# Optimization experiments

Measured on AMD Instinct MI355X. Metric: run time of the kernel, lower is better.

The kernel has to match this reference:

```python
import jax, jax.numpy as jnp
import numpy as np

EMBED = 1024
HEADS = 16
HEAD_DIM = EMBED // HEADS
HIDDEN = 4096
EPS = 1e-5


def setup_inputs() -> dict:
    key = jax.random.key(0)
    ks = jax.random.split(key, 12)
    s_e = 1.0 / np.sqrt(EMBED)
    s_h = 1.0 / np.sqrt(HIDDEN)
    inp = {
        'x': jax.random.normal(ks[0], (2, 2048, EMBED), jnp.float32),
        'Wq': jax.random.uniform(ks[1], (EMBED, EMBED), jnp.float32, -s_e, s_e),
        'bq': jnp.zeros((EMBED,), jnp.float32),
        'Wk': jax.random.uniform(ks[2], (EMBED, EMBED), jnp.float32, -s_e, s_e),
        'bk': jnp.zeros((EMBED,), jnp.float32),
        'Wv': jax.random.uniform(ks[3], (EMBED, EMBED), jnp.float32, -s_e, s_e),
        'bv': jnp.zeros((EMBED,), jnp.float32),
        'Wo': jax.random.uniform(ks[4], (EMBED, EMBED), jnp.float32, -s_e, s_e),
        'bo': jnp.zeros((EMBED,), jnp.float32),
        'g1': jnp.ones((EMBED,), jnp.float32),
        'b1': jnp.zeros((EMBED,), jnp.float32),
        'W1': jax.random.uniform(ks[5], (EMBED, HIDDEN), jnp.float32, -s_e, s_e),
        'bm1': jnp.zeros((HIDDEN,), jnp.float32),
        'W2': jax.random.uniform(ks[6], (HIDDEN, EMBED), jnp.float32, -s_h, s_h),
        'bm2': jnp.zeros((EMBED,), jnp.float32),
        'g2': jnp.ones((EMBED,), jnp.float32),
        'b2': jnp.zeros((EMBED,), jnp.float32),
    }
    return inp


def _layernorm(x, g, b):
    mu = jnp.mean(x, axis=-1, keepdims=True)
    var = jnp.mean(jnp.square(x - mu), axis=-1, keepdims=True)
    return (x - mu) * jax.lax.rsqrt(var + EPS) * g + b


def _attention(x, Wq, bq, Wk, bk, Wv, bv, Wo, bo):
    b, n, d = x.shape
    def split(h):  # [b,n,d] -> [b,H,n,hd]
        return h.reshape(b, n, HEADS, HEAD_DIM).transpose(0, 2, 1, 3)
    q = split(x @ Wq + bq)
    k = split(x @ Wk + bk)
    v = split(x @ Wv + bv)
    # NOTE: original multiplies by sqrt(head_dim) (bug preserved for faithfulness)
    scores = jnp.einsum('bhqd,bhkd->bhqk', q, k) * jnp.sqrt(jnp.float32(HEAD_DIM))
    causal = jnp.tril(jnp.ones((n, n), bool))
    scores = jnp.where(causal, scores, -jnp.inf)
    attn = jax.nn.softmax(scores, axis=-1)
    out = jnp.einsum('bhqk,bhkd->bhqd', attn, v)
    out = out.transpose(0, 2, 1, 3).reshape(b, n, d)
    return out @ Wo + bo


def reference(x, Wq, bq, Wk, bk, Wv, bv, Wo, bo, g1, b1, W1, bm1, W2, bm2, g2, b2):
    res1 = x
    x = _layernorm(_attention(x, Wq, bq, Wk, bk, Wv, bv, Wo, bo), g1, b1) + res1
    res2 = x
    h = jax.nn.gelu(x @ W1 + bm1, approximate=False) @ W2 + bm2
    return _layernorm(h, g2, b2) + res2
```

## Files before the change

kernel.cpp:

```cpp
#include <hip/hip_runtime.h>
#include <stdint.h>

typedef unsigned short u16;
typedef short short8 __attribute__((ext_vector_type(8)));
typedef float f32x4 __attribute__((ext_vector_type(4)));
typedef u16 u16x4 __attribute__((ext_vector_type(4)));
typedef u16 u16x8 __attribute__((ext_vector_type(8)));

#define MODE_F32  0
#define MODE_GELU 2
#define MODE_VT   4

#define QSCALE 11.5415603271f

__device__ __forceinline__ float b2f(u16 v) {
    union { uint32_t u; float f; } x; x.u = ((uint32_t)v) << 16; return x.f;
}
__device__ __forceinline__ u16 f2b(float f) {
    union { float f; uint32_t u; } x; x.f = f;
    uint32_t u = x.u;
    return (u16)((u + 0x7FFFu + ((u >> 16) & 1u)) >> 16);
}
__device__ __forceinline__ u16 f2b_trunc(float f) {
    union { float f; uint32_t u; } x; x.f = f;
    return (u16)(x.u >> 16);
}

#define ASYNC16(gp, lp)                                                        \
    __builtin_amdgcn_global_load_lds(                                          \
        (const __attribute__((address_space(1))) uint32_t*)(const void*)(gp),  \
        (__attribute__((address_space(3))) uint32_t*)(void*)(lp), 16, 0, 0)

#define MFMA16(a, b, c) __builtin_amdgcn_mfma_f32_16x16x32_bf16((a), (b), (c), 0, 0, 0)

__global__ __launch_bounds__(256) void split_f32(
    const float* __restrict__ in, u16* __restrict__ hi, u16* __restrict__ lo)
{
    const int i = (blockIdx.x * 256 + threadIdx.x) * 4;
    f32x4 v = *(const f32x4*)&in[i];
    u16x4 h, l;
    for (int k = 0; k < 4; k++) {
        h[k] = f2b(v[k]);
        l[k] = f2b(v[k] - b2f(h[k]));
    }
    *(u16x4*)&hi[i] = h;
    *(u16x4*)&lo[i] = l;
}

__global__ __launch_bounds__(256) void transpose_f32_bf16(
    const float* __restrict__ inA, u16* __restrict__ outA,
    const float* __restrict__ inB, u16* __restrict__ outB, int rows, int cols)
{
    const float* in = blockIdx.z ? inB : inA;
    u16* out = blockIdx.z ? outB : outA;
    __shared__ float t[32][33];
    const int r0 = blockIdx.y * 32, c0 = blockIdx.x * 32;
    const int tr = threadIdx.x >> 3, tc = (threadIdx.x & 7) * 4;
    f32x4 v = *(const f32x4*)&in[(size_t)(r0 + tr) * cols + c0 + tc];
    for (int i = 0; i < 4; i++) t[tr][tc + i] = v[i];
    __syncthreads();
    u16x4 ov;
    for (int i = 0; i < 4; i++) ov[i] = f2b(t[tc + i][tr]);
    *(u16x4*)&out[(size_t)(c0 + tr) * rows + r0 + tc] = ov;
}

__global__ __launch_bounds__(256) void transpose_split_f32(
    const float* __restrict__ inA, u16* __restrict__ hiA, u16* __restrict__ loA,
    const float* __restrict__ inB, u16* __restrict__ hiB, u16* __restrict__ loB,
    int rows, int cols)
{
    const float* in = blockIdx.z ? inB : inA;
    u16* hi = blockIdx.z ? hiB : hiA;
    u16* lo = blockIdx.z ? loB : loA;
    __shared__ float t[32][33];
    const int r0 = blockIdx.y * 32, c0 = blockIdx.x * 32;
    const int tr = threadIdx.x >> 3, tc = (threadIdx.x & 7) * 4;
    f32x4 v = *(const f32x4*)&in[(size_t)(r0 + tr) * cols + c0 + tc];
    for (int i = 0; i < 4; i++) t[tr][tc + i] = v[i];
    __syncthreads();
    u16x4 hv, lv;
    for (int i = 0; i < 4; i++) {
        const float f = t[tc + i][tr];
        hv[i] = f2b(f);
        lv[i] = f2b(f - b2f(hv[i]));
    }
    const size_t o = (size_t)(c0 + tr) * rows + r0 + tc;
    *(u16x4*)&hi[o] = hv;
    *(u16x4*)&lo[o] = lv;
}

__global__ __launch_bounds__(256) void gemm_qk_x3(
    const u16* __restrict__ Ahi, const u16* __restrict__ Alo,
    const u16* __restrict__ Bhi, const u16* __restrict__ Blo,
    const float* __restrict__ bq, const float* __restrict__ bk,
    u16* __restrict__ Qhi, u16* __restrict__ Qlo,
    u16* __restrict__ Khi, u16* __restrict__ Klo)
{
    const int K = 1024;
    __shared__ __align__(16) u16 SM[32768];
    u16* lAh = SM;          u16* lAl = SM + 8192;
    u16* lBh = SM + 16384;  u16* lBl = SM + 24576;

    const int tid = threadIdx.x;
    const int w = tid >> 6, lane = tid & 63;
    const int lane15 = lane & 15, q = lane >> 4;
    const int tM = blockIdx.y * 128, tN = blockIdx.x * 128;
    const int m0 = (w >> 1) * 64, n0 = (w & 1) * 64;

    f32x4 acc[4][4];
    for (int i = 0; i < 4; i++)
        for (int j = 0; j < 4; j++)
            acc[i][j] = (f32x4){0.f, 0.f, 0.f, 0.f};

    const int pa0 = 2 * w, pa1 = 2 * w + 1;
    const int srow = lane >> 2, sch = lane & 3;
    const u16* Ah = Ahi + (size_t)tM * K;
    const u16* Al = Alo + (size_t)tM * K;
    const u16* Bh = Bhi + (size_t)tN * K;
    const u16* Bl = Blo + (size_t)tN * K;
    const size_t r0 = (size_t)(pa0 * 16 + srow) * K + sch * 8;
    const size_t r1 = (size_t)(pa1 * 16 + srow) * K + sch * 8;

    ASYNC16(Ah + r0, lAh + pa0 * 512);  ASYNC16(Ah + r1, lAh + pa1 * 512);
    ASYNC16(Al + r0, lAl + pa0 * 512);  ASYNC16(Al + r1, lAl + pa1 * 512);
    ASYNC16(Bh + r0, lBh + pa0 * 512);  ASYNC16(Bh + r1, lBh + pa1 * 512);
    ASYNC16(Bl + r0, lBl + pa0 * 512);  ASYNC16(Bl + r1, lBl + pa1 * 512);

    const int NT = K / 32;
    for (int kt = 0; kt < NT; kt++) {
        __syncthreads();
        const int cb = (kt & 1) * 4096, nb = 4096 - cb;
        if (kt + 1 < NT) {
            const int k0 = (kt + 1) * 32;
            ASYNC16(Ah + r0 + k0, lAh + nb + pa0 * 512);  ASYNC16(Ah + r1 + k0, lAh + nb + pa1 * 512);
            ASYNC16(Al + r0 + k0, lAl + nb + pa0 * 512);  ASYNC16(Al + r1 + k0, lAl + nb + pa1 * 512);
            ASYNC16(Bh + r0 + k0, lBh + nb + pa0 * 512);  ASYNC16(Bh + r1 + k0, lBh + nb + pa1 * 512);
            ASYNC16(Bl + r0 + k0, lBl + nb + pa0 * 512);  ASYNC16(Bl + r1 + k0, lBl + nb + pa1 * 512);
        }
        short8 afh[4], afl[4], bfh[4], bfl[4];
        for (int i = 0; i < 4; i++) {
            const int o = cb + (m0 + i * 16 + lane15) * 32 + q * 8;
            afh[i] = *(const short8*)&lAh[o];
            afl[i] = *(const short8*)&lAl[o];
        }
        for (int j = 0; j < 4; j++) {
            const int o = cb + (n0 + j * 16 + lane15) * 32 + q * 8;
            bfh[j] = *(const short8*)&lBh[o];
            bfl[j] = *(const short8*)&lBl[o];
        }
        for (int i = 0; i < 4; i++)
            for (int j = 0; j < 4; j++) {
                acc[i][j] = MFMA16(afh[i], bfh[j], acc[i][j]);
                acc[i][j] = MFMA16(afh[i], bfl[j], acc[i][j]);
                acc[i][j] = MFMA16(afl[i], bfh[j], acc[i][j]);
            }
    }

    const bool isQ = (tN < 1024);
    u16* dhi = isQ ? Qhi : Khi;
    u16* dlo = isQ ? Qlo : Klo;
    const int cN = isQ ? tN : (tN - 1024);
    const float scl = isQ ? QSCALE : 1.0f;
    u16* sC = SM;
    for (int pass = 0; pass < 2; pass++) {
        __syncthreads();
        for (int i = 0; i < 4; i++) {
            const int rl0 = m0 + i * 16 + q * 4;
            for (int j = 0; j < 4; j++) {
                const int cl = n0 + j * 16 + lane15;
                const float bv = isQ ? bq[cN + cl] : bk[cN + cl];
                for (int r = 0; r < 4; r++) {
                    const float v = (acc[i][j][r] + bv) * scl;
                    const u16 hv = f2b(v);
                    sC[(rl0 + r) * 136 + cl] = pass == 0 ? hv : f2b(v - b2f(hv));
                }
            }
        }
        __syncthreads();
        u16* dst = pass == 0 ? dhi : dlo;
        for (int t8 = 0; t8 < 8; t8++) {
            const int rl = t8 * 16 + (tid >> 4), cl = (tid & 15) * 8;
            *(u16x8*)&dst[(size_t)(tM + rl) * 1024 + cN + cl] = *(const u16x8*)&sC[rl * 136 + cl];
        }
    }
}

__global__ __launch_bounds__(256) void gemm_bt(
    const u16* __restrict__ A, const u16* __restrict__ Bt, const float* __restrict__ bias,
    int M, int N, int K, int mode,
    float* __restrict__ outF, u16* __restrict__ outB, size_t pstride)
{
    __shared__ __align__(16) u16 SM[17408];
    u16* lA = SM;
    u16* lB = SM + 8192;

    const int tid = threadIdx.x;
    const int w = tid >> 6, lane = tid & 63;
    const int lane15 = lane & 15, q = lane >> 4;
    const int tM = blockIdx.y * 128, tN = blockIdx.x * 128;
    const int m0 = (w >> 1) * 64, n0 = (w & 1) * 64;

    const int kchunk = K / gridDim.z;
    const int koff = blockIdx.z * kchunk;
    outF += (size_t)blockIdx.z * pstride;

    f32x4 acc[4][4];
    for (int i = 0; i < 4; i++)
        for (int j = 0; j < 4; j++)
            acc[i][j] = (f32x4){0.f, 0.f, 0.f, 0.f};

    const int pa0 = 2 * w, pa1 = 2 * w + 1;
    const int srow = lane >> 2, sch = lane & 3;
    const u16* Abase = A + (size_t)tM * K + koff;
    const u16* Bbase = Bt + (size_t)tN * K + koff;
    const size_t r0 = (size_t)(pa0 * 16 + srow) * K + sch * 8;
    const size_t r1 = (size_t)(pa1 * 16 + srow) * K + sch * 8;

    ASYNC16(Abase + r0, lA + pa0 * 512);
    ASYNC16(Abase + r1, lA + pa1 * 512);
    ASYNC16(Bbase + r0, lB + pa0 * 512);
    ASYNC16(Bbase + r1, lB + pa1 * 512);

    const int NT = kchunk / 32;
    for (int kt = 0; kt < NT; kt++) {
        __syncthreads();
        const int cb = (kt & 1) * 4096, nb = 4096 - cb;
        if (kt + 1 < NT) {
            const int k0 = (kt + 1) * 32;
            ASYNC16(Abase + r0 + k0, lA + nb + pa0 * 512);
            ASYNC16(Abase + r1 + k0, lA + nb + pa1 * 512);
            ASYNC16(Bbase + r0 + k0, lB + nb + pa0 * 512);
            ASYNC16(Bbase + r1 + k0, lB + nb + pa1 * 512);
        }
        short8 af[4], bf[4];
        for (int i = 0; i < 4; i++) af[i] = *(const short8*)&lA[cb + (m0 + i * 16 + lane15) * 32 + q * 8];
        for (int j = 0; j < 4; j++) bf[j] = *(const short8*)&lB[cb + (n0 + j * 16 + lane15) * 32 + q * 8];
        for (int i = 0; i < 4; i++)
            for (int j = 0; j < 4; j++)
                acc[i][j] = MFMA16(af[i], bf[j], acc[i][j]);
    }

    if (mode == MODE_F32) {
        for (int i = 0; i < 4; i++) {
            const int rb = tM + m0 + i * 16 + q * 4;
            for (int j = 0; j < 4; j++) {
                const int col = tN + n0 + j * 16 + lane15;
                const float bv = (bias && blockIdx.z == 0) ? bias[col] : 0.f;
                for (int r = 0; r < 4; r++)
                    outF[(size_t)(rb + r) * N + col] = acc[i][j][r] + bv;
            }
        }
        return;
    }

    u16* sC = SM;
    __syncthreads();
    if (mode == MODE_GELU) {
        for (int i = 0; i < 4; i++) {
            const int rl0 = m0 + i * 16 + q * 4;
            for (int j = 0; j < 4; j++) {
                const int cl = n0 + j * 16 + lane15;
                const float bv = bias[tN + cl];
                for (int r = 0; r < 4; r++) {
                    float v = acc[i][j][r] + bv;
                    v = 0.5f * v * (1.f + erff(v * 0.70710678118f));
                    sC[(rl0 + r) * 136 + cl] = f2b(v);
                }
            }
        }
        __syncthreads();
        for (int t8 = 0; t8 < 8; t8++) {
            const int rl = t8 * 16 + (tid >> 4), cl = (tid & 15) * 8;
            *(u16x8*)&outB[(size_t)(tM + rl) * N + tN + cl] = *(const u16x8*)&sC[rl * 136 + cl];
        }
    } else {
        for (int i = 0; i < 4; i++) {
            const int rl0 = m0 + i * 16 + q * 4;
            for (int j = 0; j < 4; j++) {
                const int cl = n0 + j * 16 + lane15;
                const float bv = bias[tN + cl];
                for (int r = 0; r < 4; r++)
                    sC[cl * 136 + rl0 + r] = f2b(acc[i][j][r] + bv);
            }
        }
        __syncthreads();
        const int bb = tM >> 11, nbase = tM & 2047;
        for (int t8 = 0; t8 < 8; t8++) {
            const int cl = t8 * 16 + (tid >> 4), rl = (tid & 15) * 8;
            const int colg = tN + cl;
            u16* dst = &outB[((size_t)(bb * 16 + (colg >> 6)) * 64 + (colg & 63)) * 2048 + nbase + rl];
            *(u16x8*)dst = *(const u16x8*)&sC[cl * 136 + rl];
        }
    }
}

__global__ __launch_bounds__(256) void attn_fwd(
    const u16* __restrict__ Qhig, const u16* __restrict__ Qlog,
    const u16* __restrict__ Khig, const u16* __restrict__ Klog,
    const u16* __restrict__ Vtg, u16* __restrict__ Og)
{
    __shared__ u16 lQh[2][2048], lQl[2][2048];
    __shared__ u16 lKh[2][2][1024], lKl[2][2][1024];
    __shared__ u16 lV[2][2048];

    const int tid = threadIdx.x, w = tid >> 6, lane = tid & 63;
    const int lane15 = lane & 15, q = lane >> 4;
    const int bh = blockIdx.x & 31;
    const int qb = 31 - (blockIdx.x >> 5);
    const int b = bh >> 4, h = bh & 15;

    const size_t xoff = (size_t)b * 2048 * 1024 + h * 64;
    const u16* Qh_ = Qhig + xoff;
    const u16* Ql_ = Qlog + xoff;
    const u16* Kh_ = Khig + xoff;
    const u16* Kl_ = Klog + xoff;
    const u16* Vbh = Vtg + (size_t)bh * 64 * 2048;
    u16* Obh = Og + xoff;

    u16* lP = &lQh[0][0] + w * 640;

    const int srow = lane >> 2, sch = lane & 3;
    const float NEG = -3.0e38f;
    const int qrow0 = qb * 64;
    const int wrow0 = qrow0 + w * 16;
    const int ntiles = 2 * qb + 2;

    short8 ones;
    for (int i = 0; i < 8; i++) ones[i] = (short)0x3F80;

    for (int ii = 0; ii < 4; ii++) {
        const int id = w * 4 + ii;
        const int idq = id & 7, ks = idq >> 2, p = idq & 3;
        const size_t so = (size_t)(qrow0 + p * 16 + srow) * 1024 + ks * 32 + sch * 8;
        if (id < 8) ASYNC16(Qh_ + so, &lQh[ks][p * 512]);
        else        ASYNC16(Ql_ + so, &lQl[ks][p * 512]);
    }
    for (int ii = 0; ii < 3; ii++) {
        const int id = w * 3 + ii;
        if (id < 8) {
            const int sel = id >> 2, idk = id & 3, ks = idk >> 1, hh = idk & 1;
            const size_t so = (size_t)(hh * 16 + srow) * 1024 + ks * 32 + sch * 8;
            if (sel == 0) ASYNC16(Kh_ + so, &lKh[0][ks][hh * 512]);
            else          ASYNC16(Kl_ + so, &lKl[0][ks][hh * 512]);
        } else {
            const int p = id - 8;
            ASYNC16(Vbh + (size_t)(p * 16 + srow) * 2048 + sch * 8, &lV[0][p * 512]);
        }
    }

    f32x4 o[4];
    for (int j = 0; j < 4; j++) o[j] = (f32x4){0.f, 0.f, 0.f, 0.f};
    float mrow[4], lrow[4];
    for (int r = 0; r < 4; r++) { mrow[r] = NEG; lrow[r] = 0.f; }
    short8 aqh0 = {}, aqh1 = {}, aql0 = {}, aql1 = {};

    for (int t = 0; t < ntiles; t++) {
        __syncthreads();
        const int cur = t & 1, nxt = cur ^ 1;
        if (t == 0) {
            const int o0 = (w * 16 + lane15) * 32 + q * 8;
            aqh0 = *(const short8*)&lQh[0][o0];
            aqh1 = *(const short8*)&lQh[1][o0];
            aql0 = *(const short8*)&lQl[0][o0];
            aql1 = *(const short8*)&lQl[1][o0];
            __syncthreads();
        }
        if (t + 1 < ntiles) {
            const int kk1 = (t + 1) * 32;
            for (int ii = 0; ii < 3; ii++) {
                const int id = w * 3 + ii;
                if (id < 8) {
                    const int sel = id >> 2, idk = id & 3, ks = idk >> 1, hh = idk & 1;
                    const size_t so = (size_t)(kk1 + hh * 16 + srow) * 1024 + ks * 32 + sch * 8;
                    if (sel == 0) ASYNC16(Kh_ + so, &lKh[nxt][ks][hh * 512]);
                    else          ASYNC16(Kl_ + so, &lKl[nxt][ks][hh * 512]);
                } else {
                    const int p = id - 8;
                    ASYNC16(Vbh + (size_t)(p * 16 + srow) * 2048 + kk1 + sch * 8,
                            &lV[nxt][p * 512]);
                }
            }
        }
        const int kk0 = t * 32;
        if (kk0 > wrow0 + 15) continue;

        f32x4 s[2];
        for (int sub = 0; sub < 2; sub++) {
            const int ko = (sub * 16 + lane15) * 32 + q * 8;
            short8 bkh0 = *(const short8*)&lKh[cur][0][ko];
            short8 bkh1 = *(const short8*)&lKh[cur][1][ko];
            short8 bkl0 = *(const short8*)&lKl[cur][0][ko];
            short8 bkl1 = *(const short8*)&lKl[cur][1][ko];
            f32x4 z = (f32x4){0.f, 0.f, 0.f, 0.f};
            z = MFMA16(aqh0, bkh0, z);
            z = MFMA16(aqh1, bkh1, z);
            z = MFMA16(aqh0, bkl0, z);
            z = MFMA16(aqh1, bkl1, z);
            z = MFMA16(aql0, bkh0, z);
            z = MFMA16(aql1, bkh1, z);
            s[sub] = z;
        }
        const int rbase = wrow0 + q * 4;
        if (kk0 + 31 > wrow0) {
            for (int sub = 0; sub < 2; sub++)
                for (int r = 0; r < 4; r++) {
                    const int key = kk0 + sub * 16 + lane15;
                    if (key > rbase + r) s[sub][r] = NEG;
                }
        }
        float mx[4];
        for (int r = 0; r < 4; r++) mx[r] = fmaxf(s[0][r], s[1][r]);
        for (int d = 1; d < 16; d <<= 1)
            for (int r = 0; r < 4; r++) mx[r] = fmaxf(mx[r], __shfl_xor(mx[r], d));
        float alpha[4];
        for (int r = 0; r < 4; r++) {
            const float mnew = fmaxf(mrow[r], mx[r]);
            alpha[r] = __builtin_exp2f(mrow[r] - mnew);
            mrow[r] = mnew;
        }
        for (int sub = 0; sub < 2; sub++)
            for (int r = 0; r < 4; r++) {
                const float p = __builtin_exp2f(s[sub][r] - mrow[r]);
                lP[(q * 4 + r) * 40 + sub * 16 + lane15] = f2b_trunc(p);
            }
        short8 ap = *(const short8*)&lP[lane15 * 40 + q * 8];
        f32x4 zs = (f32x4){0.f, 0.f, 0.f, 0.f};
        zs = MFMA16(ap, ones, zs);
        for (int r = 0; r < 4; r++) lrow[r] = lrow[r] * alpha[r] + zs[r];
        for (int j = 0; j < 4; j++)
            for (int r = 0; r < 4; r++) o[j][r] *= alpha[r];
        for (int j = 0; j < 4; j++) {
            short8 bv = *(const short8*)&lV[cur][(j * 16 + lane15) * 32 + q * 8];
            o[j] = MFMA16(ap, bv, o[j]);
        }
    }
    float inv[4];
    for (int r = 0; r < 4; r++) inv[r] = 1.0f / lrow[r];
    for (int j = 0; j < 4; j++)
        for (int r = 0; r < 4; r++)
            Obh[(size_t)(qrow0 + w * 16 + q * 4 + r) * 1024 + j * 16 + lane15] =
                f2b(o[j][r] * inv[r]);
}

__global__ __launch_bounds__(256) void ln_res(
    const float* __restrict__ Xa, const float* __restrict__ Xb,
    const float* __restrict__ resF, const u16* __restrict__ resB,
    const float* __restrict__ g, const float* __restrict__ bb,
    u16* __restrict__ outB, float* __restrict__ outF)
{
    const int w = threadIdx.x >> 6, lane = threadIdx.x & 63;
    const int row = blockIdx.x * 4 + w;
    const size_t rowo = (size_t)row * 1024;
    f32x4 v[4];
    float s = 0.f, ss = 0.f;
    for (int i = 0; i < 4; i++) {
        const int c0 = (i * 64 + lane) * 4;
        v[i] = *(const f32x4*)&Xa[rowo + c0];
        if (Xb) {
            f32x4 v2 = *(const f32x4*)&Xb[rowo + c0];
            for (int k = 0; k < 4; k++) v[i][k] += v2[k];
        }
        for (int k = 0; k < 4; k++) { s += v[i][k]; ss += v[i][k] * v[i][k]; }
    }
    for (int d = 1; d < 64; d <<= 1) { s += __shfl_xor(s, d); ss += __shfl_xor(ss, d); }
    const float mu = s * (1.f / 1024.f);
    const float var = ss * (1.f / 1024.f) - mu * mu;
    const float rstd = rsqrtf(var + 1e-5f);
    for (int i = 0; i < 4; i++) {
        const int c0 = (i * 64 + lane) * 4;
        f32x4 gv = *(const f32x4*)&g[c0];
        f32x4 bv = *(const f32x4*)&bb[c0];
        f32x4 rv;
        if (resF) rv = *(const f32x4*)&resF[rowo + c0];
        else {
            u16x4 rb = *(const u16x4*)&resB[rowo + c0];
            for (int k = 0; k < 4; k++) rv[k] = b2f(rb[k]);
        }
        f32x4 ov;
        for (int k = 0; k < 4; k++)
            ov[k] = (v[i][k] - mu) * rstd * gv[k] + bv[k] + rv[k];
        if (outF) *(f32x4*)&outF[rowo + c0] = ov;
        if (outB) {
            u16x4 ob;
            for (int k = 0; k < 4; k++) ob[k] = f2b(ov[k]);
            *(u16x4*)&outB[rowo + c0] = ob;
        }
    }
}

extern "C" void kernel_launch(void* const* d_in, const int* in_sizes, int n_in,
                              void* d_out, int out_size, void* d_ws, size_t ws_size,
                              hipStream_t stream)
{
    const float* x   = (const float*)d_in[0];
    const float* Wq  = (const float*)d_in[1];  const float* bq  = (const float*)d_in[2];
    const float* Wk  = (const float*)d_in[3];  const float* bk  = (const float*)d_in[4];
    const float* Wv  = (const float*)d_in[5];  const float* bv  = (const float*)d_in[6];
    const float* Wo  = (const float*)d_in[7];  const float* bo  = (const float*)d_in[8];
    const float* g1  = (const float*)d_in[9];  const float* b1  = (const float*)d_in[10];
    const float* W1  = (const float*)d_in[11]; const float* bm1 = (const float*)d_in[12];
    const float* W2  = (const float*)d_in[13]; const float* bm2 = (const float*)d_in[14];
    const float* g2  = (const float*)d_in[15]; const float* b2  = (const float*)d_in[16];

    const size_t MB = (size_t)1 << 20;
    char* ws = (char*)d_ws;
    u16* xhi    = (u16*)(ws + 0 * MB);
    u16* xlo    = (u16*)(ws + 8 * MB);
    u16* WqkThi = (u16*)(ws + 16 * MB);
    u16* WqkTlo = (u16*)(ws + 20 * MB);
    u16* WvT    = (u16*)(ws + 24 * MB);
    u16* WoT    = (u16*)(ws + 26 * MB);
    u16* W1T    = (u16*)(ws + 32 * MB);
    u16* W2T    = (u16*)(ws + 40 * MB);
    u16* Qhi    = (u16*)(ws + 48 * MB);
    u16* Qlo    = (u16*)(ws + 56 * MB);
    u16* Khi    = (u16*)(ws + 64 * MB);
    u16* Klo    = (u16*)(ws + 72 * MB);
    u16* Vtb    = (u16*)(ws + 80 * MB);
    u16* aout   = (u16*)(ws + 16 * MB);
    float* O1   = (float*)(ws + 48 * MB);
    float* O2   = (float*)(ws + 64 * MB);
    u16* x1b    = (u16*)(ws + 80 * MB);
    u16* Hb     = (u16*)(ws + 0 * MB);
    float* H2a  = (float*)(ws + 48 * MB);
    float* H2b  = (float*)(ws + 64 * MB);

    split_f32<<<4096, 256, 0, stream>>>(x, xhi, xlo);
    transpose_split_f32<<<dim3(32, 32, 2), 256, 0, stream>>>(
        Wq, WqkThi, WqkTlo,
        Wk, WqkThi + 1024 * 1024, WqkTlo + 1024 * 1024, 1024, 1024);
    transpose_f32_bf16<<<dim3(32, 32, 2), 256, 0, stream>>>(Wv, WvT, Wo, WoT, 1024, 1024);
    transpose_f32_bf16<<<dim3(128, 32), 256, 0, stream>>>(W1, W1T, nullptr, nullptr, 1024, 4096);
    transpose_f32_bf16<<<dim3(32, 128), 256, 0, stream>>>(W2, W2T, nullptr, nullptr, 4096, 1024);

    gemm_qk_x3<<<dim3(16, 32), 256, 0, stream>>>(xhi, xlo, WqkThi, WqkTlo, bq, bk,
                                                 Qhi, Qlo, Khi, Klo);
    gemm_bt<<<dim3(8, 32), 256, 0, stream>>>(xhi, WvT, bv, 4096, 1024, 1024,
                                             MODE_VT, nullptr, Vtb, 0);

    attn_fwd<<<dim3(1024), 256, 0, stream>>>(Qhi, Qlo, Khi, Klo, Vtb, aout);

    gemm_bt<<<dim3(8, 32, 2), 256, 0, stream>>>(aout, WoT, bo, 4096, 1024, 1024,
                                                MODE_F32, O1, nullptr, (size_t)16 * MB / 4);
    ln_res<<<1024, 256, 0, stream>>>(O1, O2, x, nullptr, g1, b1, x1b, nullptr);

    gemm_bt<<<dim3(32, 32), 256, 0, stream>>>(x1b, W1T, bm1, 4096, 4096, 1024,
                                              MODE_GELU, nullptr, Hb, 0);
    gemm_bt<<<dim3(8, 32, 2), 256, 0, stream>>>(Hb, W2T, bm2, 4096, 1024, 4096,
                                                MODE_F32, H2a, nullptr, (size_t)16 * MB / 4);
    ln_res<<<1024, 256, 0, stream>>>(H2a, H2b, nullptr, x1b, g2, b2, nullptr, (float*)d_out);
}
```

Baseline: 472.0 us.

## Use 8 waves per 128x128 GEMM tile and interleave attention block order

Both GEMM kernels now launch 512 threads per block, each wave owning a 32x64 sub-tile instead of 64x64. The global-to-LDS staging is redistributed across the eight waves. This halves accumulator registers per thread and doubles the waves available to hide latency, at the cost of more LDS fragment reads per MFMA. Separately, attention blocks alternate long and short causal query rows so heavy and light work items are interleaved across the grid, aiming at better load balance.

```diff
diff --git a/kernel.cpp b/kernel.cpp
--- a/kernel.cpp
+++ b/kernel.cpp
@@ -89,7 +89,7 @@
     *(u16x4*)&lo[o] = lv;
 }
 
-__global__ __launch_bounds__(256) void gemm_qk_x3(
+__global__ __launch_bounds__(512) void gemm_qk_x3(
     const u16* __restrict__ Ahi, const u16* __restrict__ Alo,
     const u16* __restrict__ Bhi, const u16* __restrict__ Blo,
     const float* __restrict__ bq, const float* __restrict__ bk,
@@ -105,26 +105,30 @@
     const int w = tid >> 6, lane = tid & 63;
     const int lane15 = lane & 15, q = lane >> 4;
     const int tM = blockIdx.y * 128, tN = blockIdx.x * 128;
-    const int m0 = (w >> 1) * 64, n0 = (w & 1) * 64;
-
-    f32x4 acc[4][4];
-    for (int i = 0; i < 4; i++)
+    const int m0 = (w >> 1) * 32, n0 = (w & 1) * 64;
+
+    f32x4 acc[2][4];
+    for (int i = 0; i < 2; i++)
         for (int j = 0; j < 4; j++)
             acc[i][j] = (f32x4){0.f, 0.f, 0.f, 0.f};
 
-    const int pa0 = 2 * w, pa1 = 2 * w + 1;
     const int srow = lane >> 2, sch = lane & 3;
     const u16* Ah = Ahi + (size_t)tM * K;
     const u16* Al = Alo + (size_t)tM * K;
     const u16* Bh = Bhi + (size_t)tN * K;
     const u16* Bl = Blo + (size_t)tN * K;
-    const size_t r0 = (size_t)(pa0 * 16 + srow) * K + sch * 8;
-    const size_t r1 = (size_t)(pa1 * 16 + srow) * K + sch * 8;
-
-    ASYNC16(Ah + r0, lAh + pa0 * 512);  ASYNC16(Ah + r1, lAh + pa1 * 512);
-    ASYNC16(Al + r0, lAl + pa0 * 512);  ASYNC16(Al + r1, lAl + pa1 * 512);
-    ASYNC16(Bh + r0, lBh + pa0 * 512);  ASYNC16(Bh + r1, lBh + pa1 * 512);
-    ASYNC16(Bl + r0, lBl + pa0 * 512);  ASYNC16(Bl + r1, lBl + pa1 * 512);
+    const size_t roff = (size_t)((w * 4) & 7) * 16 * K;
+
+    #define STAGE_QK(buf_off, k0)                                              \
+        for (int ii = 0; ii < 4; ii++) {                                       \
+            const int id = w * 4 + ii, op = id >> 3, ch = id & 7;              \
+            const u16* src = op == 0 ? Ah : op == 1 ? Al : op == 2 ? Bh : Bl;  \
+            u16* dst = op == 0 ? lAh : op == 1 ? lAl : op == 2 ? lBh : lBl;    \
+            ASYNC16(src + (size_t)(ch * 16 + srow) * K + (k0) + sch * 8,       \
+                    dst + (buf_off) + ch * 512);                               \
+        }
+
+    STAGE_QK(0, 0)
 
     const int NT = K / 32;
     for (int kt = 0; kt < NT; kt++) {
@@ -132,13 +136,10 @@
         const int cb = (kt & 1) * 4096, nb = 4096 - cb;
         if (kt + 1 < NT) {
             const int k0 = (kt + 1) * 32;
-            ASYNC16(Ah + r0 + k0, lAh + nb + pa0 * 512);  ASYNC16(Ah + r1 + k0, lAh + nb + pa1 * 512);
-            ASYNC16(Al + r0 + k0, lAl + nb + pa0 * 512);  ASYNC16(Al + r1 + k0, lAl + nb + pa1 * 512);
-            ASYNC16(Bh + r0 + k0, lBh + nb + pa0 * 512);  ASYNC16(Bh + r1 + k0, lBh + nb + pa1 * 512);
-            ASYNC16(Bl + r0 + k0, lBl + nb + pa0 * 512);  ASYNC16(Bl + r1 + k0, lBl + nb + pa1 * 512);
-        }
-        short8 afh[4], afl[4], bfh[4], bfl[4];
-        for (int i = 0; i < 4; i++) {
+            STAGE_QK(nb, k0)
+        }
+        short8 afh[2], afl[2], bfh[4], bfl[4];
+        for (int i = 0; i < 2; i++) {
             const int o = cb + (m0 + i * 16 + lane15) * 32 + q * 8;
             afh[i] = *(const short8*)&lAh[o];
             afl[i] = *(const short8*)&lAl[o];
@@ -148,7 +149,7 @@
             bfh[j] = *(const short8*)&lBh[o];
             bfl[j] = *(const short8*)&lBl[o];
         }
-        for (int i = 0; i < 4; i++)
+        for (int i = 0; i < 2; i++)
             for (int j = 0; j < 4; j++) {
                 acc[i][j] = MFMA16(afh[i], bfh[j], acc[i][j]);
                 acc[i][j] = MFMA16(afh[i], bfl[j], acc[i][j]);
@@ -164,7 +165,7 @@
     u16* sC = SM;
     for (int pass = 0; pass < 2; pass++) {
         __syncthreads();
-        for (int i = 0; i < 4; i++) {
+        for (int i = 0; i < 2; i++) {
             const int rl0 = m0 + i * 16 + q * 4;
             for (int j = 0; j < 4; j++) {
                 const int cl = n0 + j * 16 + lane15;
@@ -178,14 +179,14 @@
         }
         __syncthreads();
         u16* dst = pass == 0 ? dhi : dlo;
-        for (int t8 = 0; t8 < 8; t8++) {
-            const int rl = t8 * 16 + (tid >> 4), cl = (tid & 15) * 8;
+        for (int t8 = 0; t8 < 4; t8++) {
+            const int rl = t8 * 32 + (tid >> 4), cl = (tid & 15) * 8;
             *(u16x8*)&dst[(size_t)(tM + rl) * 1024 + cN + cl] = *(const u16x8*)&sC[rl * 136 + cl];
         }
     }
 }
 
-__global__ __launch_bounds__(256) void gemm_bt(
+__global__ __launch_bounds__(512) void gemm_bt(
     const u16* __restrict__ A, const u16* __restrict__ Bt, const float* __restrict__ bias,
     int M, int N, int K, int mode,
     float* __restrict__ outF, u16* __restrict__ outB, size_t pstride)
@@ -198,28 +199,31 @@
     const int w = tid >> 6, lane = tid & 63;
     const int lane15 = lane & 15, q = lane >> 4;
     const int tM = blockIdx.y * 128, tN = blockIdx.x * 128;
-    const int m0 = (w >> 1) * 64, n0 = (w & 1) * 64;
+    const int m0 = (w >> 1) * 32, n0 = (w & 1) * 64;
 
     const int kchunk = K / gridDim.z;
     const int koff = blockIdx.z * kchunk;
     outF += (size_t)blockIdx.z * pstride;
 
-    f32x4 acc[4][4];
-    for (int i = 0; i < 4; i++)
+    f32x4 acc[2][4];
+    for (int i = 0; i < 2; i++)
         for (int j = 0; j < 4; j++)
             acc[i][j] = (f32x4){0.f, 0.f, 0.f, 0.f};
 
-    const int pa0 = 2 * w, pa1 = 2 * w + 1;
     const int srow = lane >> 2, sch = lane & 3;
     const u16* Abase = A + (size_t)tM * K + koff;
     const u16* Bbase = Bt + (size_t)tN * K + koff;
-    const size_t r0 = (size_t)(pa0 * 16 + srow) * K + sch * 8;
-    const size_t r1 = (size_t)(pa1 * 16 + srow) * K + sch * 8;
-
-    ASYNC16(Abase + r0, lA + pa0 * 512);
-    ASYNC16(Abase + r1, lA + pa1 * 512);
-    ASYNC16(Bbase + r0, lB + pa0 * 512);
-    ASYNC16(Bbase + r1, lB + pa1 * 512);
+    #define STAGE_BT(buf_off, k0)                                              \
+        for (int ii = 0; ii < 2; ii++) {                                       \
+            const int id = w * 2 + ii;                                         \
+            const u16* src = id < 8 ? Abase : Bbase;                           \
+            u16* dst = id < 8 ? lA : lB;                                       \
+            const int ch = id & 7;                                             \
+            ASYNC16(src + (size_t)(ch * 16 + srow) * K + (k0) + sch * 8,       \
+                    dst + (buf_off) + ch * 512);                               \
+        }
+
+    STAGE_BT(0, 0)
 
     const int NT = kchunk / 32;
     for (int kt = 0; kt < NT; kt++) {
@@ -227,21 +231,18 @@
         const int cb = (kt & 1) * 4096, nb = 4096 - cb;
         if (kt + 1 < NT) {
             const int k0 = (kt + 1) * 32;
-            ASYNC16(Abase + r0 + k0, lA + nb + pa0 * 512);
-            ASYNC16(Abase + r1 + k0, lA + nb + pa1 * 512);
-            ASYNC16(Bbase + r0 + k0, lB + nb + pa0 * 512);
-            ASYNC16(Bbase + r1 + k0, lB + nb + pa1 * 512);
-        }
-        short8 af[4], bf[4];
-        for (int i = 0; i < 4; i++) af[i] = *(const short8*)&lA[cb + (m0 + i * 16 + lane15) * 32 + q * 8];
+            STAGE_BT(nb, k0)
+        }
+        short8 af[2], bf[4];
+        for (int i = 0; i < 2; i++) af[i] = *(const short8*)&lA[cb + (m0 + i * 16 + lane15) * 32 + q * 8];
         for (int j = 0; j < 4; j++) bf[j] = *(const short8*)&lB[cb + (n0 + j * 16 + lane15) * 32 + q * 8];
-        for (int i = 0; i < 4; i++)
+        for (int i = 0; i < 2; i++)
             for (int j = 0; j < 4; j++)
                 acc[i][j] = MFMA16(af[i], bf[j], acc[i][j]);
     }
 
     if (mode == MODE_F32) {
-        for (int i = 0; i < 4; i++) {
+        for (int i = 0; i < 2; i++) {
             const int rb = tM + m0 + i * 16 + q * 4;
             for (int j = 0; j < 4; j++) {
                 const int col = tN + n0 + j * 16 + lane15;
@@ -256,7 +257,7 @@
     u16* sC = SM;
     __syncthreads();
     if (mode == MODE_GELU) {
-        for (int i = 0; i < 4; i++) {
+        for (int i = 0; i < 2; i++) {
             const int rl0 = m0 + i * 16 + q * 4;
             for (int j = 0; j < 4; j++) {
                 const int cl = n0 + j * 16 + lane15;
@@ -269,12 +270,12 @@
             }
         }
         __syncthreads();
-        for (int t8 = 0; t8 < 8; t8++) {
-            const int rl = t8 * 16 + (tid >> 4), cl = (tid & 15) * 8;
+        for (int t8 = 0; t8 < 4; t8++) {
+            const int rl = t8 * 32 + (tid >> 4), cl = (tid & 15) * 8;
             *(u16x8*)&outB[(size_t)(tM + rl) * N + tN + cl] = *(const u16x8*)&sC[rl * 136 + cl];
         }
     } else {
-        for (int i = 0; i < 4; i++) {
+        for (int i = 0; i < 2; i++) {
             const int rl0 = m0 + i * 16 + q * 4;
             for (int j = 0; j < 4; j++) {
                 const int cl = n0 + j * 16 + lane15;
@@ -285,8 +286,8 @@
         }
         __syncthreads();
         const int bb = tM >> 11, nbase = tM & 2047;
-        for (int t8 = 0; t8 < 8; t8++) {
-            const int cl = t8 * 16 + (tid >> 4), rl = (tid & 15) * 8;
+        for (int t8 = 0; t8 < 4; t8++) {
+            const int cl = t8 * 32 + (tid >> 4), rl = (tid & 15) * 8;
             const int colg = tN + cl;
             u16* dst = &outB[((size_t)(bb * 16 + (colg >> 6)) * 64 + (colg & 63)) * 2048 + nbase + rl];
             *(u16x8*)dst = *(const u16x8*)&sC[cl * 136 + rl];
@@ -306,7 +307,8 @@
     const int tid = threadIdx.x, w = tid >> 6, lane = tid & 63;
     const int lane15 = lane & 15, q = lane >> 4;
     const int bh = blockIdx.x & 31;
-    const int qb = 31 - (blockIdx.x >> 5);
+    const int u = blockIdx.x >> 5;
+    const int qb = (u & 1) ? (u >> 1) : (31 - (u >> 1));
     const int b = bh >> 4, h = bh & 15;
 
     const size_t xoff = (size_t)b * 2048 * 1024 + h * 64;
@@ -533,20 +535,20 @@
     transpose_f32_bf16<<<dim3(128, 32), 256, 0, stream>>>(W1, W1T, nullptr, nullptr, 1024, 4096);
     transpose_f32_bf16<<<dim3(32, 128), 256, 0, stream>>>(W2, W2T, nullptr, nullptr, 4096, 1024);
 
-    gemm_qk_x3<<<dim3(16, 32), 256, 0, stream>>>(xhi, xlo, WqkThi, WqkTlo, bq, bk,
+    gemm_qk_x3<<<dim3(16, 32), 512, 0, stream>>>(xhi, xlo, WqkThi, WqkTlo, bq, bk,
                                                  Qhi, Qlo, Khi, Klo);
-    gemm_bt<<<dim3(8, 32), 256, 0, stream>>>(xhi, WvT, bv, 4096, 1024, 1024,
+    gemm_bt<<<dim3(8, 32), 512, 0, stream>>>(xhi, WvT, bv, 4096, 1024, 1024,
                                              MODE_VT, nullptr, Vtb, 0);
 
     attn_fwd<<<dim3(1024), 256, 0, stream>>>(Qhi, Qlo, Khi, Klo, Vtb, aout);
 
-    gemm_bt<<<dim3(8, 32, 2), 256, 0, stream>>>(aout, WoT, bo, 4096, 1024, 1024,
+    gemm_bt<<<dim3(8, 32, 2), 512, 0, stream>>>(aout, WoT, bo, 4096, 1024, 1024,
                                                 MODE_F32, O1, nullptr, (size_t)16 * MB / 4);
     ln_res<<<1024, 256, 0, stream>>>(O1, O2, x, nullptr, g1, b1, x1b, nullptr);
 
-    gemm_bt<<<dim3(32, 32), 256, 0, stream>>>(x1b, W1T, bm1, 4096, 4096, 1024,
+    gemm_bt<<<dim3(32, 32), 512, 0, stream>>>(x1b, W1T, bm1, 4096, 4096, 1024,
                                               MODE_GELU, nullptr, Hb, 0);
-    gemm_bt<<<dim3(8, 32, 2), 256, 0, stream>>>(Hb, W2T, bm2, 4096, 1024, 4096,
+    gemm_bt<<<dim3(8, 32, 2), 512, 0, stream>>>(Hb, W2T, bm2, 4096, 1024, 4096,
                                                 MODE_F32, H2a, nullptr, (size_t)16 * MB / 4);
     ln_res<<<1024, 256, 0, stream>>>(H2a, H2b, nullptr, x1b, g2, b2, nullptr, (float*)d_out);
 }
```

Result: faster. 446.0 us (-5.5%).
